# Performance work log

Hardware: AMD Instinct MI355X
Metric: run time of the kernel (lower is better)

The kernel has to match this reference:

```python
import jax, jax.numpy as jnp
import numpy as np
from jax import lax

K = 100
NUM_CLASSES = 80
MIN_X = 1; MIN_Y = 1; MAX_X = 4; MAX_Y = 4   # int(base_layer_range/16) for [16,64,16,64]
KEEP = 300
IOU_TH = 0.5
ROI_H = 2 * MAX_Y + 1  # 9
ROI_W = 2 * MAX_X + 1  # 9
MASK_OUT = 36          # 9 -> two stride-2 deconvs -> 36
SCALE = (36.0 - 1.0) / (9.0 - 1.0)
BN_INV = 1.0 / np.sqrt(1.0 + 1e-3)  # BN eval, running mean 0 / var 1, eps=1e-3
SIZES = [(64, 64), (32, 32), (16, 16)]


def bilinear(img, xx, yy):
    # img [..., H, W]; xx, yy same shape S; border-clamped bilinear sample -> [..., *S]
    H, W = img.shape[-2], img.shape[-1]
    xx = jnp.clip(xx, 0.0, W - 1.0)
    yy = jnp.clip(yy, 0.0, H - 1.0)
    x0f = jnp.floor(xx); y0f = jnp.floor(yy)
    wx = xx - x0f; wy = yy - y0f
    x0 = x0f.astype(jnp.int32); y0 = y0f.astype(jnp.int32)
    x1 = jnp.minimum(x0 + 1, W - 1); y1 = jnp.minimum(y0 + 1, H - 1)
    v00 = img[..., y0, x0]; v01 = img[..., y0, x1]
    v10 = img[..., y1, x0]; v11 = img[..., y1, x1]
    return (1 - wy) * ((1 - wx) * v00 + wx * v01) + wy * ((1 - wx) * v10 + wx * v11)


def roi_align(feat, boxes):
    # feat [C,H,W], boxes [N,4] in feat coords -> [N,C,ROI_H,ROI_W] (sampling_ratio=1)
    n = boxes.shape[0]
    x1, y1, x2, y2 = boxes[:, 0], boxes[:, 1], boxes[:, 2], boxes[:, 3]
    jx = (jnp.arange(ROI_W, dtype=jnp.float32) + 0.5) / ROI_W
    jy = (jnp.arange(ROI_H, dtype=jnp.float32) + 0.5) / ROI_H
    gx = x1[:, None] + (x2 - x1)[:, None] * jx  # [N,ROI_W]
    gy = y1[:, None] + (y2 - y1)[:, None] * jy  # [N,ROI_H]
    xx = jnp.broadcast_to(gx[:, None, :], (n, ROI_H, ROI_W))
    yy = jnp.broadcast_to(gy[:, :, None], (n, ROI_H, ROI_W))
    out = bilinear(feat, xx, yy)  # [C,N,ROI_H,ROI_W]
    return jnp.transpose(out, (1, 0, 2, 3))


def crop_resize(masks, boxes):
    # masks [N,h,w], boxes [N,4] -> [N,MASK_OUT,MASK_OUT]
    n = boxes.shape[0]
    t = jnp.arange(MASK_OUT, dtype=jnp.float32) / (MASK_OUT - 1.0)
    x1, y1, x2, y2 = boxes[:, 0], boxes[:, 1], boxes[:, 2], boxes[:, 3]
    gx = x1[:, None] + (x2 - x1)[:, None] * t
    gy = y1[:, None] + (y2 - y1)[:, None] * t
    xx = jnp.broadcast_to(gx[:, None, :], (n, MASK_OUT, MASK_OUT))
    yy = jnp.broadcast_to(gy[:, :, None], (n, MASK_OUT, MASK_OUT))
    return jax.vmap(bilinear)(masks, xx, yy)


def nms_keep(boxes, scores):
    # greedy NMS, faithful to torchvision semantics; returns bool keep flags [N]
    n = boxes.shape[0]
    x1, y1, x2, y2 = boxes[:, 0], boxes[:, 1], boxes[:, 2], boxes[:, 3]
    area = (x2 - x1) * (y2 - y1)
    ix1 = jnp.maximum(x1[:, None], x1[None, :]); iy1 = jnp.maximum(y1[:, None], y1[None, :])
    ix2 = jnp.minimum(x2[:, None], x2[None, :]); iy2 = jnp.minimum(y2[:, None], y2[None, :])
    inter = jnp.clip(ix2 - ix1, 0.0) * jnp.clip(iy2 - iy1, 0.0)
    iou = inter / (area[:, None] + area[None, :] - inter + 1e-9)
    order = jnp.argsort(-scores)  # stable
    def step(carry, idx):
        supp, keep = carry
        k = jnp.logical_not(supp[idx])
        keep = keep.at[idx].set(k)
        supp = jnp.logical_or(supp, jnp.logical_and(k, iou[idx] > IOU_TH))
        return (supp, keep), None
    init = (jnp.zeros((n,), bool), jnp.zeros((n,), bool))
    (_, keep), _ = lax.scan(step, init, order)
    return keep


def _conv(x, w, b, pad):
    y = lax.conv_general_dilated(x, w, (1, 1), [(pad, pad), (pad, pad)],
                                 dimension_numbers=('NCHW', 'OIHW', 'NCHW'))
    return y + b[None, :, None, None]


def _deconv(x, w, b):
    # ConvTranspose2d(k=2, s=2): fractionally-strided conv, doubles spatial size
    y = lax.conv_general_dilated(x, w, (1, 1), [(1, 1), (1, 1)], lhs_dilation=(2, 2),
                                 dimension_numbers=('NCHW', 'OIHW', 'NCHW'))
    return y + b[None, :, None, None]


def _bn(x, g, b):
    return x * (g * BN_INV)[None, :, None, None] + b[None, :, None, None]


def mask_head(x, c1_w, c1_b, mid_w, mid_b, bn_g, bn_b, d1_w, d1_b, d2_w, d2_b, c5_w, c5_b, c6_w, c6_b):
    r = jax.nn.relu
    h = r(_bn(_conv(x, c1_w, c1_b, 1), bn_g[0], bn_b[0]))
    for j in range(3):  # conv2..conv4
        h = r(_bn(_conv(h, mid_w[j], mid_b[j], 1), bn_g[1 + j], bn_b[1 + j]))
    h = r(_deconv(h, d1_w, d1_b))
    h = r(_bn(_conv(h, c5_w, c5_b, 1), bn_g[4], bn_b[4]))
    h = r(_deconv(h, d2_w, d2_b))
    return jax.nn.sigmoid(_conv(h, c6_w, c6_b, 0))


def _decode_layer(heat, tlr, brr, i, H0, W0):
    C, H, W = heat.shape
    hw = H * W
    scores, inds = lax.top_k(heat.reshape(-1), K)
    clses = (inds // hw).astype(jnp.float32)
    rem = inds % hw
    ys = (rem // W).astype(jnp.float32)
    xs = (rem % W).astype(jnp.float32)
    t = tlr.reshape(2, hw)[:, rem]  # [2,K]
    b = brr.reshape(2, hw)[:, rem]
    rx = float(MAX_X - MIN_X); ry = float(MAX_Y - MIN_Y)
    cx = (MAX_X + MIN_X) / 2.0;  cy = (MAX_Y + MIN_Y) / 2.0
    tlx = jnp.clip(xs - (rx * t[0] + cx), 0.0, float(W))
    tly = jnp.clip(ys - (ry * t[1] + cy), 0.0, float(H))
    brx = jnp.clip(xs + (rx * b[0] + cx), 0.0, float(W))
    bry = jnp.clip(ys + (ry * b[1] + cy), 0.0, float(H))
    boxes = jnp.stack([tlx, tly, brx, bry], 1)
    sc = jnp.where((brx < tlx) | (bry < tly), -1.0, scores)
    mb = jnp.stack([xs - MAX_X, ys - MAX_Y, xs + MAX_X, ys + MAX_Y,
                    jnp.full((K,), float(i))], 1)
    s2, order = lax.top_k(sc, K)  # num_dets(1000) >= K -> full sort by score
    boxes = boxes[order]; mb = mb[order]; cls = clses[order]
    lay = jnp.full((K,), float(i))
    cols = jnp.stack([s2, s2, lay, cls], 1)
    bws = jnp.concatenate([boxes, cols], 1)  # boxes_without_scaling [K,8]
    scale = jnp.array([W0 / W, H0 / H, W0 / W, H0 / H], jnp.float32)
    dets = jnp.concatenate([boxes * scale, cols], 1)
    return dets, bws, mb


def _decode_one(h0, h1, h2, t0, t1, t2, b0, b1, b2, f0, f1, f2,
                c1_w, c1_b, mid_w, mid_b, bn_g, bn_b, d1_w, d1_b, d2_w, d2_b,
                c5_w, c5_b, c6_w, c6_b):
    heats = (h0, h1, h2); tls = (t0, t1, t2); brs = (b0, b1, b2); feats = (f0, f1, f2)
    H0, W0 = heats[0].shape[1], heats[0].shape[2]
    dets_l, bws_l, mb_l = [], [], []
    for i in range(3):
        d, bw, mb = _decode_layer(heats[i], tls[i], brs[i], i, H0, W0)
        dets_l.append(d); bws_l.append(bw); mb_l.append(mb)
    dets = jnp.concatenate(dets_l, 0)   # [300,8]
    bws = jnp.concatenate(bws_l, 0)
    mb = jnp.concatenate(mb_l, 0)       # [300,5]
    # NMS faithful to source: boxes = detections[:,1:5], scores = detections[:,4]
    keep = nms_keep(dets[:, 1:5], dets[:, 4])
    sel = jnp.argsort(-jnp.where(keep, dets[:, 4], -1e9))[:KEEP]
    dets = dets[sel]; bws = bws[sel]; mb = mb[sel]
    # sort by mask layer index descending (features processed last->first)
    ord2 = jnp.argsort(-mb[:, 4])
    dets = dets[ord2]; bws = bws[ord2]; mb = mb[ord2]
    # ROI pool each box from its own layer's feature map
    pooled = jnp.stack([roi_align(feats[i], mb[:, :4]) for i in range(3)], 0)  # [3,N,C,9,9]
    lay = jnp.clip(mb[:, 4].astype(jnp.int32), 0, 2)
    rois = pooled[lay, jnp.arange(KEEP)]  # [N,256,9,9]
    masks_all = mask_head(rois, c1_w, c1_b, mid_w, mid_b, bn_g, bn_b,
                          d1_w, d1_b, d2_w, d2_b, c5_w, c5_b, c6_w, c6_b)  # [N,80,36,36]
    cls = jnp.clip(dets[:, 7].astype(jnp.int32), 0, NUM_CLASSES - 1)
    masks = masks_all[jnp.arange(KEEP), cls]  # [N,36,36] (one-hot scatter/select)
    bws4 = bws[:, :4] - jnp.tile(mb[:, :2], (1, 2))
    norm_boxes = SCALE * bws4
    masks = crop_resize(masks, norm_boxes)
    return dets, masks


def setup_inputs():
    key = jax.random.key(0)
    ks = jax.random.split(key, 32)
    B = 1
    inp = {}
    for i, (H, W) in enumerate(SIZES):
        inp['heat%d' % i] = jax.random.uniform(ks[i], (B, NUM_CLASSES, H, W), jnp.float32)
        inp['tl%d' % i] = 0.1 * jax.random.normal(ks[3 + i], (B, 2, H, W), jnp.float32)
        inp['br%d' % i] = 0.1 * jax.random.normal(ks[6 + i], (B, 2, H, W), jnp.float32)
        inp['feat%d' % i] = jax.random.normal(ks[9 + i], (B, 256, H, W), jnp.float32)
    inp['c1_w'] = 0.05 * jax.random.normal(ks[12], (256, 256, 3, 3), jnp.float32)
    inp['c1_b'] = jnp.zeros((256,), jnp.float32)
    inp['mid_w'] = 0.05 * jax.random.normal(ks[13], (3, 256, 256, 3, 3), jnp.float32)
    inp['mid_b'] = jnp.zeros((3, 256), jnp.float32)
    inp['bn_g'] = jnp.ones((5, 256), jnp.float32)
    inp['bn_b'] = jnp.zeros((5, 256), jnp.float32)
    inp['d1_w'] = 0.05 * jax.random.normal(ks[14], (256, 256, 2, 2), jnp.float32)
    inp['d1_b'] = jnp.zeros((256,), jnp.float32)
    inp['d2_w'] = 0.05 * jax.random.normal(ks[15], (256, 256, 2, 2), jnp.float32)
    inp['d2_b'] = jnp.zeros((256,), jnp.float32)
    inp['c5_w'] = 0.05 * jax.random.normal(ks[16], (256, 256, 3, 3), jnp.float32)
    inp['c5_b'] = jnp.zeros((256,), jnp.float32)
    inp['c6_w'] = 0.05 * jax.random.normal(ks[17], (NUM_CLASSES, 256, 1, 1), jnp.float32)
    inp['c6_b'] = jnp.zeros((NUM_CLASSES,), jnp.float32)
    return inp


def reference(heat0, heat1, heat2, tl0, tl1, tl2, br0, br1, br2, feat0, feat1, feat2,
              c1_w, c1_b, mid_w, mid_b, bn_g, bn_b, d1_w, d1_b, d2_w, d2_b,
              c5_w, c5_b, c6_w, c6_b):
    dets, masks = jax.vmap(_decode_one, in_axes=(0,) * 12 + (None,) * 14)(
        heat0, heat1, heat2, tl0, tl1, tl2, br0, br1, br2, feat0, feat1, feat2,
        c1_w, c1_b, mid_w, mid_b, bn_g, bn_b, d1_w, d1_b, d2_w, d2_b, c5_w, c5_b, c6_w, c6_b)
    return dets, masks  # [B,300,8], [B,300,36,36]
```

## Files before the change

### kernel.cpp

```cpp
#include <hip/hip_runtime.h>
#include <math.h>

typedef __attribute__((ext_vector_type(8))) short bf16x8;
typedef __attribute__((ext_vector_type(4))) float f32x4;

__device__ __forceinline__ unsigned fkey_u(float v){
  unsigned b = __float_as_uint(v);
  return (b & 0x80000000u) ? ~b : (b | 0x80000000u);
}
__device__ __forceinline__ float fkey_inv(unsigned m){
  unsigned b = (m & 0x80000000u) ? (m & 0x7fffffffu) : ~m;
  return __uint_as_float(b);
}
__device__ __forceinline__ unsigned short f2bf(float f){
  unsigned u = __float_as_uint(f);
  unsigned r = (u + 0x7fffu + ((u>>16)&1u)) >> 16;
  return (unsigned short)r;
}
__device__ __forceinline__ unsigned long long shfl_xor_u64(unsigned long long v, int mask){
  int lo = __shfl_xor((int)(unsigned)(v & 0xFFFFFFFFull), mask, 64);
  int hi = __shfl_xor((int)(unsigned)(v >> 32), mask, 64);
  return ((unsigned long long)(unsigned)hi << 32) | (unsigned long long)(unsigned)lo;
}
#define BNI 0.9995003746877732f

template<int E, int J>
__device__ __forceinline__ void reg_step(unsigned long long* key, int t, int k2){
  #pragma unroll
  for (int r=0;r<E;r++){
    if ((r & J)==0){
      int e = t*E + r;
      bool desc = ((e & k2)==0);
      unsigned long long a=key[r], b=key[r^J];
      if (desc ? (a<b) : (a>b)){ key[r]=b; key[r^J]=a; }
    }
  }
}
template<int E>
__device__ __forceinline__ void reg_tail(unsigned long long* key, int t, int k2, int jstart){
  if constexpr (E>=8) { if (jstart>=4) reg_step<E,4>(key,t,k2); }
  if constexpr (E>=4) { if (jstart>=2) reg_step<E,2>(key,t,k2); }
  if (jstart>=1) reg_step<E,1>(key,t,k2);
}
template<int E>
__device__ void bitonic_desc(unsigned long long* key, unsigned long long* lds){
  const int t = threadIdx.x;
  const int N = E*256;
  for (int k2=2;k2<=N;k2<<=1){
    for (int j=k2>>1; j>=E; j>>=1){
      int w = j/E;
      bool lower = ((t & w)==0);
      bool desc  = (((t*E) & k2)==0);
      bool keep_max = (desc == lower);
      if (w < 64){
        #pragma unroll
        for (int r=0;r<E;r++){
          unsigned long long mine=key[r];
          unsigned long long o=shfl_xor_u64(mine, w);
          bool gt = mine > o;
          key[r] = keep_max ? (gt?mine:o) : (gt?o:mine);
        }
      } else {
        __syncthreads();
        #pragma unroll
        for (int r=0;r<E;r++) lds[t*E+r]=key[r];
        __syncthreads();
        #pragma unroll
        for (int r=0;r<E;r++){
          unsigned long long mine=key[r];
          unsigned long long o=lds[(t*E+r)^j];
          bool gt = mine > o;
          key[r] = keep_max ? (gt?mine:o) : (gt?o:mine);
        }
      }
    }
    int jstart = ((k2>>1) < (E>>1)) ? (k2>>1) : (E>>1);
    reg_tail<E>(key,t,k2,jstart);
  }
  __syncthreads();
  #pragma unroll
  for (int r=0;r<E;r++) lds[t*E+r]=key[r];
  __syncthreads();
}

__global__ __launch_bounds__(256) void k_sel1(
    const float* __restrict__ h0, const float* __restrict__ h1, const float* __restrict__ h2,
    unsigned long long* __restrict__ c1)
{
  int b = blockIdx.x;
  int layer, chunk;
  if (b < 320){ layer=0; chunk=b; }
  else if (b < 400){ layer=1; chunk=b-320; }
  else { layer=2; chunk=b-400; }
  const float* heat = (layer==0)?h0:((layer==1)?h1:h2);
  __shared__ unsigned long long lds[1024];
  unsigned long long key[4];
  int t = threadIdx.x;
  int base = chunk*1024 + t*4;
  float4 v = *(const float4*)(heat + base);
  key[0] = ((unsigned long long)fkey_u(v.x)<<32) | (unsigned long long)(0xFFFFFFFFu - (unsigned)(base+0));
  key[1] = ((unsigned long long)fkey_u(v.y)<<32) | (unsigned long long)(0xFFFFFFFFu - (unsigned)(base+1));
  key[2] = ((unsigned long long)fkey_u(v.z)<<32) | (unsigned long long)(0xFFFFFFFFu - (unsigned)(base+2));
  key[3] = ((unsigned long long)fkey_u(v.w)<<32) | (unsigned long long)(0xFFFFFFFFu - (unsigned)(base+3));
  bitonic_desc<4>(key, lds);
  if (t<100) c1[(size_t)b*100 + t] = lds[t];
}

__global__ __launch_bounds__(256) void k_sel2(
    const unsigned long long* __restrict__ c1, unsigned long long* __restrict__ c2)
{
  int b = blockIdx.x;
  __shared__ unsigned long long lds[2048];
  unsigned long long key[8];
  int t=threadIdx.x;
  const unsigned long long* src = c1 + (size_t)b*2000;
  #pragma unroll
  for (int r=0;r<8;r++){
    int i=t*8+r;
    key[r] = (i<2000)? src[i] : 0ull;
  }
  bitonic_desc<8>(key, lds);
  if (t<100) c2[(size_t)b*100+t]=lds[t];
}

__global__ __launch_bounds__(256) void k_sel3_decode(
    const unsigned long long* __restrict__ c2,
    const float* __restrict__ tl0,const float* __restrict__ tl1,const float* __restrict__ tl2,
    const float* __restrict__ br0,const float* __restrict__ br1,const float* __restrict__ br2,
    float* __restrict__ dets, float* __restrict__ bws, float* __restrict__ mbw)
{
  int layer = blockIdx.x;
  int hw = 4096 >> (layer*2);
  int W = 64>>layer;
  float Wf = (float)W;
  const float* tl = (layer==0)?tl0:((layer==1)?tl1:tl2);
  const float* br = (layer==0)?br0:((layer==1)?br1:br2);
  int base = (layer==0)?0:((layer==1)?1600:2000);
  int cnt  = (layer==0)?1600:((layer==1)?400:100);
  __shared__ unsigned long long lds[2048];
  __shared__ float scl[100];
  unsigned long long key[8];
  int t = threadIdx.x;
  #pragma unroll
  for (int r=0;r<8;r++){
    int i=t*8+r;
    key[r] = (i<cnt)? c2[base+i] : 0ull;
  }
  bitonic_desc<8>(key, lds);
  unsigned long long kwin=0;
  if (t<100) kwin = lds[t];
  float tlx=0,tly=0,brx=0,bry=0,xs=0,ys=0,clsfv=0,scv=0;
  if (t<100){
    unsigned m=(unsigned)(kwin>>32);
    unsigned gidx = 0xFFFFFFFFu - (unsigned)(kwin & 0xFFFFFFFFull);
    float val = fkey_inv(m);
    int cls = (int)(gidx / (unsigned)hw);
    int rem = (int)(gidx % (unsigned)hw);
    int iy = rem / W, ix = rem % W;
    xs = (float)ix; ys = (float)iy; clsfv = (float)cls;
    float t0=tl[rem], t1=tl[hw+rem], b0=br[rem], b1=br[hw+rem];
    tlx = fminf(fmaxf(xs - (3.0f*t0 + 2.5f), 0.0f), Wf);
    tly = fminf(fmaxf(ys - (3.0f*t1 + 2.5f), 0.0f), Wf);
    brx = fminf(fmaxf(xs + (3.0f*b0 + 2.5f), 0.0f), Wf);
    bry = fminf(fmaxf(ys + (3.0f*b1 + 2.5f), 0.0f), Wf);
    scv = ((brx<tlx)||(bry<tly)) ? -1.0f : val;
    scl[t]=scv;
  }
  __syncthreads();
  if (t<100){
    int rank=0;
    for (int i=0;i<100;i++){
      float si=scl[i];
      rank += ((si>scv)||(si==scv && i<t)) ? 1 : 0;
    }
    int row = layer*100 + rank;
    float sx = (float)(1<<layer);
    float* dr = dets + row*8;
    dr[0]=tlx*sx; dr[1]=tly*sx; dr[2]=brx*sx; dr[3]=bry*sx;
    dr[4]=scv; dr[5]=scv; dr[6]=(float)layer; dr[7]=clsfv;
    float* bwr = bws + row*8;
    bwr[0]=tlx;bwr[1]=tly;bwr[2]=brx;bwr[3]=bry;bwr[4]=scv;bwr[5]=scv;bwr[6]=(float)layer;bwr[7]=clsfv;
    float* mr = mbw + row*5;
    mr[0]=xs-4.0f; mr[1]=ys-4.0f; mr[2]=xs+4.0f; mr[3]=ys+4.0f; mr[4]=(float)layer;
  }
}

#define SCAN_GROUP(SW, BASE, CNT) \
  _Pragma("unroll 4") \
  for (int rr=0; rr<CNT; rr++){ \
    int r = BASE+rr; \
    unsigned long long w0=sm[r][0],w1=sm[r][1],w2=sm[r][2],w3=sm[r][3],w4=sm[r][4]; \
    unsigned long long kq = (~(SW>>rr))&1ull; \
    keepr[r]=(unsigned char)kq; \
    unsigned long long msk = 0ull - kq; \
    s0|=w0&msk; s1|=w1&msk; s2|=w2&msk; s3|=w3&msk; s4|=w4&msk; \
  }

__global__ __launch_bounds__(320) void k_nms(
    const float* __restrict__ dets, const float* __restrict__ bws, const float* __restrict__ mbw,
    float* __restrict__ out_dets, float* __restrict__ mbf, int* __restrict__ clsf,
    int* __restrict__ layf, float* __restrict__ nbox)
{
  __shared__ __align__(16) float4 rb[300];
  __shared__ float rs[300];
  __shared__ int orig[300];
  __shared__ __align__(16) float sc[300];
  __shared__ __align__(16) float kk[300];
  __shared__ __align__(16) float lq[300];
  __shared__ float lyv[300];
  __shared__ unsigned long long sm[300][5];
  __shared__ unsigned char keepr[304];
  __shared__ int sel_[300], fperm[300];
  int t = threadIdx.x;
  float X1=0,Y1=0,X2=0,Y2=0,S=0;
  if (t<300){
    const float* r = dets + t*8;
    X1=r[1];Y1=r[2];X2=r[3];Y2=r[4];
    S=r[4];
    sc[t]=S;
    lyv[t]=mbw[t*5+4];
  }
  __syncthreads();
  if (t<300){
    int rank=0;
    for (int j4=0;j4<75;j4++){
      float4 s4=*(const float4*)&sc[j4*4];
      int j=j4*4;
      rank += ((s4.x>S)||(s4.x==S&&(j+0)<t)) ? 1:0;
      rank += ((s4.y>S)||(s4.y==S&&(j+1)<t)) ? 1:0;
      rank += ((s4.z>S)||(s4.z==S&&(j+2)<t)) ? 1:0;
      rank += ((s4.w>S)||(s4.w==S&&(j+3)<t)) ? 1:0;
    }
    rb[rank]=make_float4(X1,Y1,X2,Y2);
    rs[rank]=S;
    orig[rank]=t;
  }
  __syncthreads();
  if (t<300){
    float4 me=rb[t];
    float A=(me.z-me.x)*(me.w-me.y);
    #pragma unroll
    for (int jw=0;jw<5;jw++){
      unsigned long long bits=0;
      int lim=(jw==4)?44:64;
      for (int jj=0;jj<lim;jj++){
        int j=jw*64+jj;
        float4 q=rb[j];
        float aj=(q.z-q.x)*(q.w-q.y);
        float ix1=fmaxf(me.x,q.x), iy1=fmaxf(me.y,q.y);
        float ix2=fminf(me.z,q.z), iy2=fminf(me.w,q.w);
        float it=fmaxf(ix2-ix1,0.f)*fmaxf(iy2-iy1,0.f);
        float iou=it/(A+aj-it+1e-9f);
        bits |= ((unsigned long long)(iou>0.5f))<<jj;
      }
      sm[t][jw]=bits;
    }
  }
  __syncthreads();
  if (t==0){
    unsigned long long s0=0,s1=0,s2=0,s3=0,s4=0;
    SCAN_GROUP(s0,0,64)
    SCAN_GROUP(s1,64,64)
    SCAN_GROUP(s2,128,64)
    SCAN_GROUP(s3,192,64)
    SCAN_GROUP(s4,256,44)
  }
  __syncthreads();
  if (t<300) kk[orig[t]] = keepr[t] ? rs[t] : -1000000000.0f;
  __syncthreads();
  float KV=0; int rank2=0;
  if (t<300){
    KV=kk[t];
    for (int j4=0;j4<75;j4++){
      float4 s4=*(const float4*)&kk[j4*4];
      int j=j4*4;
      rank2 += ((s4.x>KV)||(s4.x==KV&&(j+0)<t)) ? 1:0;
      rank2 += ((s4.y>KV)||(s4.y==KV&&(j+1)<t)) ? 1:0;
      rank2 += ((s4.z>KV)||(s4.z==KV&&(j+2)<t)) ? 1:0;
      rank2 += ((s4.w>KV)||(s4.w==KV&&(j+3)<t)) ? 1:0;
    }
    sel_[rank2]=t;
  }
  __syncthreads();
  if (t<300) lq[t]=lyv[sel_[t]];
  __syncthreads();
  if (t<300){
    float L=lq[t]; int rank3=0;
    for (int j4=0;j4<75;j4++){
      float4 s4=*(const float4*)&lq[j4*4];
      int j=j4*4;
      rank3 += ((s4.x>L)||(s4.x==L&&(j+0)<t)) ? 1:0;
      rank3 += ((s4.y>L)||(s4.y==L&&(j+1)<t)) ? 1:0;
      rank3 += ((s4.z>L)||(s4.z==L&&(j+2)<t)) ? 1:0;
      rank3 += ((s4.w>L)||(s4.w==L&&(j+3)<t)) ? 1:0;
    }
    fperm[rank3]=sel_[t];
  }
  __syncthreads();
  if (t<300){
    int src=fperm[t];
    const float* dr=dets+src*8;
    #pragma unroll
    for (int c=0;c<8;c++) out_dets[t*8+c]=dr[c];
    const float* mr=mbw+src*5;
    #pragma unroll
    for (int c=0;c<5;c++) mbf[t*5+c]=mr[c];
    int cc=(int)dr[7]; cc = cc<0?0:(cc>79?79:cc); clsf[t]=cc;
    int lv=(int)mr[4]; lv = lv<0?0:(lv>2?2:lv); layf[t]=lv;
    const float* bw=bws+src*8;
    nbox[t*4+0]=4.375f*(bw[0]-mr[0]);
    nbox[t*4+1]=4.375f*(bw[1]-mr[1]);
    nbox[t*4+2]=4.375f*(bw[2]-mr[0]);
    nbox[t*4+3]=4.375f*(bw[3]-mr[1]);
  }
}

__global__ __launch_bounds__(256) void k_roi(
    const float* __restrict__ f0,const float* __restrict__ f1,const float* __restrict__ f2,
    const float* __restrict__ mbf, const int* __restrict__ layf,
    unsigned short* __restrict__ rois, int r0)
{
  int nl = blockIdx.x; int g = r0 + nl;
  __shared__ int ix0[9], ix1[9], iy0[9], iy1[9];
  __shared__ float wx[9], wy[9];
  int lay = layf[g];
  int W = 64>>lay;
  float Wf1 = (float)(W-1);
  const float* feat = (lay==0)?f0:((lay==1)?f1:f2);
  int t=threadIdx.x;
  if (t<9){
    float x1=mbf[g*5+0], x2=mbf[g*5+2];
    float jx = ((float)t + 0.5f)/9.0f;
    float gx = x1 + (x2-x1)*jx;
    float xx = fminf(fmaxf(gx,0.0f), Wf1);
    float x0f = floorf(xx);
    wx[t]=xx-x0f;
    int x0=(int)x0f; ix0[t]=x0; ix1[t]=min(x0+1,W-1);
  } else if (t>=16 && t<25){
    int j=t-16;
    float y1=mbf[g*5+1], y2=mbf[g*5+3];
    float jy=((float)j+0.5f)/9.0f;
    float gy=y1+(y2-y1)*jy;
    float yy=fminf(fmaxf(gy,0.0f),Wf1);
    float y0f=floorf(yy);
    wy[j]=yy-y0f;
    int y0=(int)y0f; iy0[j]=y0; iy1[j]=min(y0+1,W-1);
  }
  __syncthreads();
  int c=t;
  const float* fp = feat + (size_t)c*W*W;
  unsigned short* op = rois + (size_t)nl*81*256;
  for (int p=0;p<81;p++){
    int py=p/9, px=p%9;
    float v00=fp[iy0[py]*W+ix0[px]];
    float v01=fp[iy0[py]*W+ix1[px]];
    float v10=fp[iy1[py]*W+ix0[px]];
    float v11=fp[iy1[py]*W+ix1[px]];
    float wxx=wx[px], wyy=wy[py];
    float v = (1.0f-wyy)*((1.0f-wxx)*v00 + wxx*v01) + wyy*((1.0f-wxx)*v10 + wxx*v11);
    op[(size_t)p*256 + c] = f2bf(v);
  }
}

__global__ __launch_bounds__(64) void k_wprep3(
    const float* __restrict__ c1w, const float* __restrict__ midw, const float* __restrict__ c5w,
    unsigned short* __restrict__ WB)
{
  int b = blockIdx.x, c = blockIdx.y, l = threadIdx.x;
  int t = b>>7;
  const float* src = (c==0)? c1w : (c<=3 ? midw + (size_t)(c-1)*589824 : c5w);
  unsigned short* dst = WB + (size_t)c*589824 + ((size_t)b<<9) + l*8;
  int co = (b&15)*16 + (l&15);
  int cib = ((b>>4)&7)*32 + ((l>>4)<<3);
  #pragma unroll
  for (int j=0;j<8;j++) dst[j] = f2bf(src[((size_t)co*256 + cib + j)*9 + t]);
}
__global__ __launch_bounds__(64) void k_wprep2(
    const float* __restrict__ d1w, const float* __restrict__ d2w,
    unsigned short* __restrict__ WD)
{
  int b = blockIdx.x, c = blockIdx.y, l = threadIdx.x;
  int t = b>>7;
  const float* src = (c==0)? d1w : d2w;
  unsigned short* dst = WD + (size_t)c*262144 + ((size_t)b<<9) + l*8;
  int co = (b&15)*16 + (l&15);
  int cib = ((b>>4)&7)*32 + ((l>>4)<<3);
  #pragma unroll
  for (int j=0;j<8;j++) dst[j] = f2bf(src[((size_t)co*256 + cib + j)*4 + t]);
}

__global__ __launch_bounds__(256,3) void k_mconv9h(
    const unsigned short* __restrict__ Xg, unsigned short* __restrict__ Yg,
    const unsigned short* __restrict__ WBc,
    const float* __restrict__ Bc, const float* __restrict__ Gg, const float* __restrict__ Bn)
{
  __shared__ __align__(16) unsigned short Xp[88*264];
  int tid=threadIdx.x, l=tid&63, w=tid>>6;
  int h=blockIdx.y;
  int rlo = h ? 4 : -1;
  const unsigned short* Xr = Xg + (size_t)blockIdx.x*81*256;
  for (int idx=tid; idx<88*32; idx+=256){
    int pp=idx>>5, k8=idx&31;
    int y=pp/11 + rlo, x=pp%11 - 1;
    uint4 v{0,0,0,0};
    if ((unsigned)y<9u && (unsigned)x<9u) v = *(const uint4*)(Xr + ((y*9+x)<<8) + (k8<<3));
    *(uint4*)&Xp[pp*264 + (k8<<3)] = v;
  }
  __syncthreads();
  int mbase = h*48;
  int pixb[3];
  #pragma unroll
  for (int mt=0;mt<3;mt++){
    int m=mbase+mt*16+(l&15); if(m>80)m=80;
    pixb[mt]=(m/9 - rlo)*11 + (m%9) + 1;
  }
  int kg=(l>>4)<<3;
  f32x4 acc[3][4] = {};
  const unsigned short* wbase = WBc + (size_t)l*8;
  for (int t9=0;t9<9;t9++){
    int toff=(t9/3-1)*11 + (t9%3-1);
    for (int kc=0;kc<8;kc++){
      bf16x8 a[3], b[4];
      #pragma unroll
      for (int mt=0;mt<3;mt++) a[mt] = *(const bf16x8*)&Xp[(pixb[mt]+toff)*264 + (kc<<5) + kg];
      #pragma unroll
      for (int nn=0;nn<4;nn++) b[nn] = *(const bf16x8*)(wbase + ((size_t)(((t9<<3)+kc)*16 + (w<<2)+nn)<<9));
      #pragma unroll
      for (int mt=0;mt<3;mt++){
        #pragma unroll
        for (int nn=0;nn<4;nn++)
          acc[mt][nn] = __builtin_amdgcn_mfma_f32_16x16x32_bf16(a[mt], b[nn], acc[mt][nn], 0,0,0);
      }
    }
  }
  unsigned short* Yr = Yg + (size_t)blockIdx.x*81*256;
  int rb=(l>>4)<<2;
  #pragma unroll
  for (int nn=0;nn<4;nn++){
    int co=(w<<6)+(nn<<4)+(l&15);
    float bc=Bc[co], gm=Gg[co]*BNI, bb=Bn[co];
    #pragma unroll
    for (int mt=0;mt<3;mt++){
      #pragma unroll
      for (int r=0;r<4;r++){
        int m=mbase+mt*16+rb+r;
        if (m<81){
          float v=fmaxf((acc[mt][nn][r]+bc)*gm+bb, 0.f);
          Yr[m*256+co]=f2bf(v);
        }
      }
    }
  }
}

__global__ __launch_bounds__(256,3) void k_mdeconv1(
    const unsigned short* __restrict__ Xg, unsigned short* __restrict__ Yg,
    const unsigned short* __restrict__ WD1, const float* __restrict__ Bd)
{
  __shared__ __align__(16) unsigned short Xp[81*264];
  int tid=threadIdx.x, l=tid&63, w=tid>>6;
  int tp=blockIdx.y;
  const unsigned short* Xr = Xg + (size_t)blockIdx.x*81*256;
  for (int idx=tid; idx<81*32; idx+=256){
    int pp=idx>>5, k8=idx&31;
    *(uint4*)&Xp[pp*264+(k8<<3)] = *(const uint4*)(Xr + (pp<<8)+(k8<<3));
  }
  __syncthreads();
  int pixb[6];
  #pragma unroll
  for (int mt=0;mt<6;mt++){ int m=mt*16+(l&15); pixb[mt]=(m>80)?80:m; }
  int kg=(l>>4)<<3;
  f32x4 acc[6][4] = {};
  const unsigned short* wbase = WD1 + (size_t)tp*65536 + (size_t)l*8;
  for (int kc=0;kc<8;kc++){
    bf16x8 a[6], b[4];
    #pragma unroll
    for (int mt=0;mt<6;mt++) a[mt] = *(const bf16x8*)&Xp[pixb[mt]*264 + (kc<<5) + kg];
    #pragma unroll
    for (int nn=0;nn<4;nn++) b[nn] = *(const bf16x8*)(wbase + ((size_t)(kc*16 + (w<<2)+nn)<<9));
    #pragma unroll
    for (int mt=0;mt<6;mt++){
      #pragma unroll
      for (int nn=0;nn<4;nn++)
        acc[mt][nn] = __builtin_amdgcn_mfma_f32_16x16x32_bf16(a[mt], b[nn], acc[mt][nn], 0,0,0);
    }
  }
  unsigned short* Yr = Yg + (size_t)blockIdx.x*324*256;
  int ky=tp>>1, kx=tp&1;
  int rb=(l>>4)<<2;
  #pragma unroll
  for (int nn=0;nn<4;nn++){
    int co=(w<<6)+(nn<<4)+(l&15);
    float bd=Bd[co];
    #pragma unroll
    for (int mt=0;mt<6;mt++){
      #pragma unroll
      for (int r=0;r<4;r++){
        int m=mt*16+rb+r;
        if (m<81){
          int iy=m/9, ix=m%9;
          int opx=(2*iy+1-ky)*18 + (2*ix+1-kx);
          Yr[opx*256+co]=f2bf(fmaxf(acc[mt][nn][r]+bd,0.f));
        }
      }
    }
  }
}

__global__ __launch_bounds__(256,3) void k_mconv18(
    const unsigned short* __restrict__ Xg, unsigned short* __restrict__ Yg,
    const unsigned short* __restrict__ WBc,
    const float* __restrict__ Bc, const float* __restrict__ Gg, const float* __restrict__ Bn)
{
  __shared__ __align__(16) unsigned short Xp[160*136];
  int tid=threadIdx.x, l=tid&63, w=tid>>6;
  int rg=blockIdx.y, ch=blockIdx.z;
  const unsigned short* Xr = Xg + (size_t)blockIdx.x*324*256;
  int pixb[7];
  #pragma unroll
  for (int mt=0;mt<7;mt++){ int m=mt*16+(l&15); if(m>107)m=107; pixb[mt]=(m/18)*20+(m%18); }
  int kg=(l>>4)<<3;
  f32x4 acc[7][2] = {};
  const unsigned short* wbase = WBc + (size_t)l*8;
  for (int h=0;h<2;h++){
    __syncthreads();
    for (int idx=tid; idx<160*16; idx+=256){
      int pp=idx>>4, k8=idx&15;
      int py=rg*6-1+pp/20, px=pp%20-1;
      uint4 v{0,0,0,0};
      if ((unsigned)py<18u && (unsigned)px<18u)
        v = *(const uint4*)(Xr + ((py*18+px)<<8) + (h<<7) + (k8<<3));
      *(uint4*)&Xp[pp*136 + (k8<<3)] = v;
    }
    __syncthreads();
    for (int t9=0;t9<9;t9++){
      int toff=(t9/3)*20 + (t9%3);
      for (int kc=0;kc<4;kc++){
        int kcg=(h<<2)+kc;
        bf16x8 a[7], b[2];
        #pragma unroll
        for (int mt=0;mt<7;mt++) a[mt] = *(const bf16x8*)&Xp[(pixb[mt]+toff)*136 + (kc<<5) + kg];
        #pragma unroll
        for (int nn=0;nn<2;nn++) b[nn] = *(const bf16x8*)(wbase + ((size_t)(((t9<<3)+kcg)*16 + (ch<<3)+(w<<1)+nn)<<9));
        #pragma unroll
        for (int mt=0;mt<7;mt++){
          #pragma unroll
          for (int nn=0;nn<2;nn++)
            acc[mt][nn] = __builtin_amdgcn_mfma_f32_16x16x32_bf16(a[mt], b[nn], acc[mt][nn], 0,0,0);
        }
      }
    }
  }
  unsigned short* Yr = Yg + (size_t)blockIdx.x*324*256;
  int rb=(l>>4)<<2;
  #pragma unroll
  for (int nn=0;nn<2;nn++){
    int co=(ch<<7)+(w<<5)+(nn<<4)+(l&15);
    float bc=Bc[co], gm=Gg[co]*BNI, bb=Bn[co];
    #pragma unroll
    for (int mt=0;mt<7;mt++){
      #pragma unroll
      for (int r=0;r<4;r++){
        int m=mt*16+rb+r;
        if (m<108){
          int opx=rg*108+m;
          Yr[opx*256+co]=f2bf(fmaxf((acc[mt][nn][r]+bc)*gm+bb, 0.f));
        }
      }
    }
  }
}

__global__ __launch_bounds__(256,2) void k_mdec2c6(
    const unsigned short* __restrict__ Xg,
    const unsigned short* __restrict__ WD2, const float* __restrict__ Bd,
    const float* __restrict__ W6, const float* __restrict__ B6,
    const int* __restrict__ clsf, float* __restrict__ mask36, int r0)
{
  __shared__ __align__(16) unsigned short Xp[108*264];
  __shared__ float part[4][112];
  int tid=threadIdx.x, l=tid&63, w=tid>>6;
  int tp=blockIdx.y, rg=blockIdx.z;
  int g=r0+blockIdx.x;
  const unsigned short* Xr = Xg + (size_t)blockIdx.x*324*256 + (size_t)rg*108*256;
  for (int idx=tid; idx<108*32; idx+=256){
    int pp=idx>>5, k8=idx&31;
    *(uint4*)&Xp[pp*264+(k8<<3)] = *(const uint4*)(Xr + (pp<<8)+(k8<<3));
  }
  __syncthreads();
  int pixb[7];
  #pragma unroll
  for (int mt=0;mt<7;mt++){ int m=mt*16+(l&15); pixb[mt]=(m>107)?107:m; }
  int kg=(l>>4)<<3;
  f32x4 acc[7][4] = {};
  const unsigned short* wbase = WD2 + (size_t)tp*65536 + (size_t)l*8;
  for (int kc=0;kc<8;kc++){
    bf16x8 a[7], b[4];
    #pragma unroll
    for (int mt=0;mt<7;mt++) a[mt] = *(const bf16x8*)&Xp[pixb[mt]*264 + (kc<<5) + kg];
    #pragma unroll
    for (int nn=0;nn<4;nn++) b[nn] = *(const bf16x8*)(wbase + ((size_t)(kc*16 + (w<<2)+nn)<<9));
    #pragma unroll
    for (int mt=0;mt<7;mt++){
      #pragma unroll
      for (int nn=0;nn<4;nn++)
        acc[mt][nn] = __builtin_amdgcn_mfma_f32_16x16x32_bf16(a[mt], b[nn], acc[mt][nn], 0,0,0);
    }
  }
  int cls=clsf[g];
  float w6v[4], bdv[4];
  #pragma unroll
  for (int nn=0;nn<4;nn++){
    int co=(w<<6)+(nn<<4)+(l&15);
    w6v[nn]=W6[(size_t)cls*256+co];
    bdv[nn]=Bd[co];
  }
  int rb=(l>>4)<<2;
  #pragma unroll
  for (int mt=0;mt<7;mt++){
    float s0=0.f,s1=0.f,s2=0.f,s3=0.f;
    #pragma unroll
    for (int nn=0;nn<4;nn++){
      s0 += fmaxf(acc[mt][nn][0]+bdv[nn],0.f)*w6v[nn];
      s1 += fmaxf(acc[mt][nn][1]+bdv[nn],0.f)*w6v[nn];
      s2 += fmaxf(acc[mt][nn][2]+bdv[nn],0.f)*w6v[nn];
      s3 += fmaxf(acc[mt][nn][3]+bdv[nn],0.f)*w6v[nn];
    }
    #pragma unroll
    for (int o=1;o<16;o<<=1){
      s0 += __shfl_xor(s0,o,64);
      s1 += __shfl_xor(s1,o,64);
      s2 += __shfl_xor(s2,o,64);
      s3 += __shfl_xor(s3,o,64);
    }
    if ((l&15)==0){
      int mb=mt*16+rb;
      part[w][mb+0]=s0; part[w][mb+1]=s1; part[w][mb+2]=s2; part[w][mb+3]=s3;
    }
  }
  __syncthreads();
  if (tid<108){
    float lg = part[0][tid]+part[1][tid]+part[2][tid]+part[3][tid] + B6[cls];
    int pg=rg*108+tid, iy=pg/18, ix=pg%18;
    int ky=tp>>1, kx=tp&1;
    mask36[(size_t)g*1296 + (2*iy+1-ky)*36 + (2*ix+1-kx)] = 1.0f/(1.0f+expf(-lg));
  }
}

__global__ __launch_bounds__(256) void k_crop(
    const float* __restrict__ mask36, const float* __restrict__ nbox,
    float* __restrict__ outm)
{
  int r=blockIdx.x;
  __shared__ float m[1296];
  int t=threadIdx.x;
  for (int i=t;i<1296;i+=256) m[i]=mask36[(size_t)r*1296+i];
  float x1=nbox[r*4+0], y1=nbox[r*4+1], x2=nbox[r*4+2], y2=nbox[r*4+3];
  __syncthreads();
  for (int p=t;p<1296;p+=256){
    int oy=p/36, ox=p%36;
    float tx=(float)ox/35.0f, ty=(float)oy/35.0f;
    float gx=x1+(x2-x1)*tx, gy=y1+(y2-y1)*ty;
    float xx=fminf(fmaxf(gx,0.f),35.0f), yy=fminf(fmaxf(gy,0.f),35.0f);
    float x0f=floorf(xx), y0f=floorf(yy);
    float wxv=xx-x0f, wyv=yy-y0f;
    int x0=(int)x0f, y0=(int)y0f;
    int x1i=min(x0+1,35), y1i=min(y0+1,35);
    float v00=m[y0*36+x0], v01=m[y0*36+x1i], v10=m[y1i*36+x0], v11=m[y1i*36+x1i];
    outm[(size_t)r*1296+p]=(1.f-wyv)*((1.f-wxv)*v00+wxv*v01)+wyv*((1.f-wxv)*v10+wxv*v11);
  }
}

extern "C" void kernel_launch(void* const* d_in, const int* in_sizes, int n_in,
                              void* d_out, int out_size, void* d_ws, size_t ws_size,
                              hipStream_t stream) {
  int iH[3], iT[3], iB[3], iF[3];
  if (n_in >= 12 && in_sizes[1] == 2*64*64) {
    for (int l=0;l<3;l++){ iH[l]=l*4+0; iT[l]=l*4+1; iB[l]=l*4+2; iF[l]=l*4+3; }
  } else {
    for (int l=0;l<3;l++){ iH[l]=l; iT[l]=3+l; iB[l]=6+l; iF[l]=9+l; }
  }
  const float* heat0=(const float*)d_in[iH[0]];
  const float* heat1=(const float*)d_in[iH[1]];
  const float* heat2=(const float*)d_in[iH[2]];
  const float* tl0=(const float*)d_in[iT[0]];
  const float* tl1=(const float*)d_in[iT[1]];
  const float* tl2=(const float*)d_in[iT[2]];
  const float* br0=(const float*)d_in[iB[0]];
  const float* br1=(const float*)d_in[iB[1]];
  const float* br2=(const float*)d_in[iB[2]];
  const float* feat0=(const float*)d_in[iF[0]];
  const float* feat1=(const float*)d_in[iF[1]];
  const float* feat2=(const float*)d_in[iF[2]];
  const float* c1w=(const float*)d_in[12];
  const float* c1b=(const float*)d_in[13];
  const float* midw=(const float*)d_in[14];
  const float* midb=(const float*)d_in[15];
  const float* bng=(const float*)d_in[16];
  const float* bnb=(const float*)d_in[17];
  const float* d1w=(const float*)d_in[18];
  const float* d1b=(const float*)d_in[19];
  const float* d2w=(const float*)d_in[20];
  const float* d2b=(const float*)d_in[21];
  const float* c5w=(const float*)d_in[22];
  const float* c5b=(const float*)d_in[23];
  const float* c6w=(const float*)d_in[24];
  const float* c6b=(const float*)d_in[25];
  float* out=(float*)d_out;

  char* ws=(char*)d_ws;
  size_t cur=0;
  auto alloc=[&](size_t bytes)->char*{
    char* p=ws+cur;
    cur=(cur+bytes+255)&~(size_t)255;
    return p;
  };
  unsigned short* WB=(unsigned short*)alloc(5ull*589824*2);
  unsigned short* WD=(unsigned short*)alloc(2ull*262144*2);
  unsigned long long* c1s=(unsigned long long*)alloc(420ull*100*8);
  unsigned long long* c2s=(unsigned long long*)alloc(21ull*100*8);
  float* detsw=(float*)alloc(300*8*4);
  float* bwsw=(float*)alloc(300*8*4);
  float* mbw=(float*)alloc(300*5*4);
  float* mbf=(float*)alloc(300*5*4);
  int* clsf=(int*)alloc(300*4);
  int* layf=(int*)alloc(300*4);
  float* nbox=(float*)alloc(300*4*4);
  float* mask36=(float*)alloc(300ull*1296*4);
  size_t fixed=cur;
  size_t perroi = (size_t)(2*81 + 2*324)*256*2;
  size_t avail = (ws_size>fixed+4096)? (ws_size-fixed-4096):0;
  int NRC = (int)(avail/perroi);
  if (NRC>300) NRC=300;
  if (NRC<1) NRC=1;
  unsigned short* X0 =(unsigned short*)alloc((size_t)NRC*81*256*2);
  unsigned short* B9 =(unsigned short*)alloc((size_t)NRC*81*256*2);
  unsigned short* C18=(unsigned short*)alloc((size_t)NRC*324*256*2);
  unsigned short* D18=(unsigned short*)alloc((size_t)NRC*324*256*2);

  k_wprep3<<<dim3(1152,5),dim3(64),0,stream>>>(c1w,midw,c5w,WB);
  k_wprep2<<<dim3(512,2),dim3(64),0,stream>>>(d1w,d2w,WD);

  k_sel1<<<dim3(420),dim3(256),0,stream>>>(heat0,heat1,heat2,c1s);
  k_sel2<<<dim3(21),dim3(256),0,stream>>>(c1s,c2s);
  k_sel3_decode<<<dim3(3),dim3(256),0,stream>>>(c2s,tl0,tl1,tl2,br0,br1,br2,detsw,bwsw,mbw);
  k_nms<<<dim3(1),dim3(320),0,stream>>>(detsw,bwsw,mbw,out,mbf,clsf,layf,nbox);

  for (int r0=0;r0<300;r0+=NRC){
    int nr = (300-r0 < NRC)? (300-r0) : NRC;
    k_roi<<<dim3(nr),dim3(256),0,stream>>>(feat0,feat1,feat2,mbf,layf,X0,r0);
    k_mconv9h<<<dim3(nr,2),dim3(256),0,stream>>>(X0,B9,WB,               c1b,       bng,      bnb);
    k_mconv9h<<<dim3(nr,2),dim3(256),0,stream>>>(B9,X0,WB+1ull*589824,   midb,      bng+256,  bnb+256);
    k_mconv9h<<<dim3(nr,2),dim3(256),0,stream>>>(X0,B9,WB+2ull*589824,   midb+256,  bng+512,  bnb+512);
    k_mconv9h<<<dim3(nr,2),dim3(256),0,stream>>>(B9,X0,WB+3ull*589824,   midb+512,  bng+768,  bnb+768);
    k_mdeconv1<<<dim3(nr,4),dim3(256),0,stream>>>(X0,C18,WD,d1b);
    k_mconv18<<<dim3(nr,3,2),dim3(256),0,stream>>>(C18,D18,WB+4ull*589824, c5b, bng+1024, bnb+1024);
    k_mdec2c6<<<dim3(nr,4,3),dim3(256),0,stream>>>(D18,WD+262144,d2b,c6w,c6b,clsf,mask36,r0);
  }
  k_crop<<<dim3(300),dim3(256),0,stream>>>(mask36,nbox,out+2400);
}
```

Baseline: 657.0 us.

## Merge deconv tap and channel-half blocks, swizzle conv18 LDS tile

The deconv1 and deconv2+c6 kernels now loop over the four deconv taps inside one block instead of launching one block per tap, so the staged input tile in LDS is reused across taps. The 18x18 conv kernel drops its output-channel-half grid dimension so each block computes all 256 channels, with more accumulators per wave. Its LDS tile now uses an XOR swizzle on 16-byte chunks to reduce bank conflicts. The trade-off is fewer blocks (lower parallelism across the GPU) and higher register pressure from the larger accumulator array.

```diff
diff --git a/kernel.cpp b/kernel.cpp
--- a/kernel.cpp
+++ b/kernel.cpp
@@ -459,7 +459,6 @@
 {
   __shared__ __align__(16) unsigned short Xp[81*264];
   int tid=threadIdx.x, l=tid&63, w=tid>>6;
-  int tp=blockIdx.y;
   const unsigned short* Xr = Xg + (size_t)blockIdx.x*81*256;
   for (int idx=tid; idx<81*32; idx+=256){
     int pp=idx>>5, k8=idx&31;
@@ -470,37 +469,39 @@
   #pragma unroll
   for (int mt=0;mt<6;mt++){ int m=mt*16+(l&15); pixb[mt]=(m>80)?80:m; }
   int kg=(l>>4)<<3;
-  f32x4 acc[6][4] = {};
-  const unsigned short* wbase = WD1 + (size_t)tp*65536 + (size_t)l*8;
-  for (int kc=0;kc<8;kc++){
-    bf16x8 a[6], b[4];
+  int rb=(l>>4)<<2;
+  unsigned short* Yr = Yg + (size_t)blockIdx.x*324*256;
+  for (int tp=0;tp<4;tp++){
+    f32x4 acc[6][4] = {};
+    const unsigned short* wbase = WD1 + (size_t)tp*65536 + (size_t)l*8;
+    for (int kc=0;kc<8;kc++){
+      bf16x8 a[6], b[4];
+      #pragma unroll
+      for (int mt=0;mt<6;mt++) a[mt] = *(const bf16x8*)&Xp[pixb[mt]*264 + (kc<<5) + kg];
+      #pragma unroll
+      for (int nn=0;nn<4;nn++) b[nn] = *(const bf16x8*)(wbase + ((size_t)(kc*16 + (w<<2)+nn)<<9));
+      #pragma unroll
+      for (int mt=0;mt<6;mt++){
+        #pragma unroll
+        for (int nn=0;nn<4;nn++)
+          acc[mt][nn] = __builtin_amdgcn_mfma_f32_16x16x32_bf16(a[mt], b[nn], acc[mt][nn], 0,0,0);
+      }
+    }
+    int ky=tp>>1, kx=tp&1;
     #pragma unroll
-    for (int mt=0;mt<6;mt++) a[mt] = *(const bf16x8*)&Xp[pixb[mt]*264 + (kc<<5) + kg];
-    #pragma unroll
-    for (int nn=0;nn<4;nn++) b[nn] = *(const bf16x8*)(wbase + ((size_t)(kc*16 + (w<<2)+nn)<<9));
-    #pragma unroll
-    for (int mt=0;mt<6;mt++){
-      #pragma unroll
-      for (int nn=0;nn<4;nn++)
-        acc[mt][nn] = __builtin_amdgcn_mfma_f32_16x16x32_bf16(a[mt], b[nn], acc[mt][nn], 0,0,0);
-    }
-  }
-  unsigned short* Yr = Yg + (size_t)blockIdx.x*324*256;
-  int ky=tp>>1, kx=tp&1;
-  int rb=(l>>4)<<2;
-  #pragma unroll
-  for (int nn=0;nn<4;nn++){
-    int co=(w<<6)+(nn<<4)+(l&15);
-    float bd=Bd[co];
-    #pragma unroll
-    for (int mt=0;mt<6;mt++){
-      #pragma unroll
-      for (int r=0;r<4;r++){
-        int m=mt*16+rb+r;
-        if (m<81){
-          int iy=m/9, ix=m%9;
-          int opx=(2*iy+1-ky)*18 + (2*ix+1-kx);
-          Yr[opx*256+co]=f2bf(fmaxf(acc[mt][nn][r]+bd,0.f));
+    for (int nn=0;nn<4;nn++){
+      int co=(w<<6)+(nn<<4)+(l&15);
+      float bd=Bd[co];
+      #pragma unroll
+      for (int mt=0;mt<6;mt++){
+        #pragma unroll
+        for (int r=0;r<4;r++){
+          int m=mt*16+rb+r;
+          if (m<81){
+            int iy=m/9, ix=m%9;
+            int opx=(2*iy+1-ky)*18 + (2*ix+1-kx);
+            Yr[opx*256+co]=f2bf(fmaxf(acc[mt][nn][r]+bd,0.f));
+          }
         }
       }
     }
@@ -514,13 +515,13 @@
 {
   __shared__ __align__(16) unsigned short Xp[160*136];
   int tid=threadIdx.x, l=tid&63, w=tid>>6;
-  int rg=blockIdx.y, ch=blockIdx.z;
+  int rg=blockIdx.y;
   const unsigned short* Xr = Xg + (size_t)blockIdx.x*324*256;
   int pixb[7];
   #pragma unroll
   for (int mt=0;mt<7;mt++){ int m=mt*16+(l&15); if(m>107)m=107; pixb[mt]=(m/18)*20+(m%18); }
-  int kg=(l>>4)<<3;
-  f32x4 acc[7][2] = {};
+  int g16=l>>4;
+  f32x4 acc[7][4] = {};
   const unsigned short* wbase = WBc + (size_t)l*8;
   for (int h=0;h<2;h++){
     __syncthreads();
@@ -530,22 +531,26 @@
       uint4 v{0,0,0,0};
       if ((unsigned)py<18u && (unsigned)px<18u)
         v = *(const uint4*)(Xr + ((py*18+px)<<8) + (h<<7) + (k8<<3));
-      *(uint4*)&Xp[pp*136 + (k8<<3)] = v;
+      *(uint4*)&Xp[pp*136 + ((k8 ^ (pp&7))<<3)] = v;
     }
     __syncthreads();
     for (int t9=0;t9<9;t9++){
       int toff=(t9/3)*20 + (t9%3);
       for (int kc=0;kc<4;kc++){
         int kcg=(h<<2)+kc;
-        bf16x8 a[7], b[2];
-        #pragma unroll
-        for (int mt=0;mt<7;mt++) a[mt] = *(const bf16x8*)&Xp[(pixb[mt]+toff)*136 + (kc<<5) + kg];
-        #pragma unroll
-        for (int nn=0;nn<2;nn++) b[nn] = *(const bf16x8*)(wbase + ((size_t)(((t9<<3)+kcg)*16 + (ch<<3)+(w<<1)+nn)<<9));
+        bf16x8 a[7], b[4];
+        #pragma unroll
+        for (int mt=0;mt<7;mt++){
+          int row=pixb[mt]+toff;
+          int gg=((kc<<2)+g16) ^ (row&7);
+          a[mt] = *(const bf16x8*)&Xp[row*136 + (gg<<3)];
+        }
+        #pragma unroll
+        for (int nn=0;nn<4;nn++) b[nn] = *(const bf16x8*)(wbase + ((size_t)(((t9<<3)+kcg)*16 + (w<<2)+nn)<<9));
         #pragma unroll
         for (int mt=0;mt<7;mt++){
           #pragma unroll
-          for (int nn=0;nn<2;nn++)
+          for (int nn=0;nn<4;nn++)
             acc[mt][nn] = __builtin_amdgcn_mfma_f32_16x16x32_bf16(a[mt], b[nn], acc[mt][nn], 0,0,0);
         }
       }
@@ -554,8 +559,8 @@
   unsigned short* Yr = Yg + (size_t)blockIdx.x*324*256;
   int rb=(l>>4)<<2;
   #pragma unroll
-  for (int nn=0;nn<2;nn++){
-    int co=(ch<<7)+(w<<5)+(nn<<4)+(l&15);
+  for (int nn=0;nn<4;nn++){
+    int co=(w<<6)+(nn<<4)+(l&15);
     float bc=Bc[co], gm=Gg[co]*BNI, bb=Bn[co];
     #pragma unroll
     for (int mt=0;mt<7;mt++){
@@ -580,7 +585,7 @@
   __shared__ __align__(16) unsigned short Xp[108*264];
   __shared__ float part[4][112];
   int tid=threadIdx.x, l=tid&63, w=tid>>6;
-  int tp=blockIdx.y, rg=blockIdx.z;
+  int rg=blockIdx.y;
   int g=r0+blockIdx.x;
   const unsigned short* Xr = Xg + (size_t)blockIdx.x*324*256 + (size_t)rg*108*256;
   for (int idx=tid; idx<108*32; idx+=256){
@@ -592,21 +597,7 @@
   #pragma unroll
   for (int mt=0;mt<7;mt++){ int m=mt*16+(l&15); pixb[mt]=(m>107)?107:m; }
   int kg=(l>>4)<<3;
-  f32x4 acc[7][4] = {};
-  const unsigned short* wbase = WD2 + (size_t)tp*65536 + (size_t)l*8;
-  for (int kc=0;kc<8;kc++){
-    bf16x8 a[7], b[4];
-    #pragma unroll
-    for (int mt=0;mt<7;mt++) a[mt] = *(const bf16x8*)&Xp[pixb[mt]*264 + (kc<<5) + kg];
-    #pragma unroll
-    for (int nn=0;nn<4;nn++) b[nn] = *(const bf16x8*)(wbase + ((size_t)(kc*16 + (w<<2)+nn)<<9));
-    #pragma unroll
-    for (int mt=0;mt<7;mt++){
-      #pragma unroll
-      for (int nn=0;nn<4;nn++)
-        acc[mt][nn] = __builtin_amdgcn_mfma_f32_16x16x32_bf16(a[mt], b[nn], acc[mt][nn], 0,0,0);
-    }
-  }
+  int rb=(l>>4)<<2;
   int cls=clsf[g];
   float w6v[4], bdv[4];
   #pragma unroll
@@ -615,35 +606,53 @@
     w6v[nn]=W6[(size_t)cls*256+co];
     bdv[nn]=Bd[co];
   }
-  int rb=(l>>4)<<2;
-  #pragma unroll
-  for (int mt=0;mt<7;mt++){
-    float s0=0.f,s1=0.f,s2=0.f,s3=0.f;
+  float b6c=B6[cls];
+  for (int tp=0;tp<4;tp++){
+    f32x4 acc[7][4] = {};
+    const unsigned short* wbase = WD2 + (size_t)tp*65536 + (size_t)l*8;
+    for (int kc=0;kc<8;kc++){
+      bf16x8 a[7], b[4];
+      #pragma unroll
+      for (int mt=0;mt<7;mt++) a[mt] = *(const bf16x8*)&Xp[pixb[mt]*264 + (kc<<5) + kg];
+      #pragma unroll
+      for (int nn=0;nn<4;nn++) b[nn] = *(const bf16x8*)(wbase + ((size_t)(kc*16 + (w<<2)+nn)<<9));
+      #pragma unroll
+      for (int mt=0;mt<7;mt++){
+        #pragma unroll
+        for (int nn=0;nn<4;nn++)
+          acc[mt][nn] = __builtin_amdgcn_mfma_f32_16x16x32_bf16(a[mt], b[nn], acc[mt][nn], 0,0,0);
+      }
+    }
     #pragma unroll
-    for (int nn=0;nn<4;nn++){
-      s0 += fmaxf(acc[mt][nn][0]+bdv[nn],0.f)*w6v[nn];
-      s1 += fmaxf(acc[mt][nn][1]+bdv[nn],0.f)*w6v[nn];
-      s2 += fmaxf(acc[mt][nn][2]+bdv[nn],0.f)*w6v[nn];
-      s3 += fmaxf(acc[mt][nn][3]+bdv[nn],0.f)*w6v[nn];
-    }
-    #pragma unroll
-    for (int o=1;o<16;o<<=1){
-      s0 += __shfl_xor(s0,o,64);
-      s1 += __shfl_xor(s1,o,64);
-      s2 += __shfl_xor(s2,o,64);
-      s3 += __shfl_xor(s3,o,64);
-    }
-    if ((l&15)==0){
-      int mb=mt*16+rb;
-      part[w][mb+0]=s0; part[w][mb+1]=s1; part[w][mb+2]=s2; part[w][mb+3]=s3;
-    }
-  }
-  __syncthreads();
-  if (tid<108){
-    float lg = part[0][tid]+part[1][tid]+part[2][tid]+part[3][tid] + B6[cls];
-    int pg=rg*108+tid, iy=pg/18, ix=pg%18;
-    int ky=tp>>1, kx=tp&1;
-    mask36[(size_t)g*1296 + (2*iy+1-ky)*36 + (2*ix+1-kx)] = 1.0f/(1.0f+expf(-lg));
+    for (int mt=0;mt<7;mt++){
+      float s0=0.f,s1=0.f,s2=0.f,s3=0.f;
+      #pragma unroll
+      for (int nn=0;nn<4;nn++){
+        s0 += fmaxf(acc[mt][nn][0]+bdv[nn],0.f)*w6v[nn];
+        s1 += fmaxf(acc[mt][nn][1]+bdv[nn],0.f)*w6v[nn];
+        s2 += fmaxf(acc[mt][nn][2]+bdv[nn],0.f)*w6v[nn];
+        s3 += fmaxf(acc[mt][nn][3]+bdv[nn],0.f)*w6v[nn];
+      }
+      #pragma unroll
+      for (int o=1;o<16;o<<=1){
+        s0 += __shfl_xor(s0,o,64);
+        s1 += __shfl_xor(s1,o,64);
+        s2 += __shfl_xor(s2,o,64);
+        s3 += __shfl_xor(s3,o,64);
+      }
+      if ((l&15)==0){
+        int mb=mt*16+rb;
+        part[w][mb+0]=s0; part[w][mb+1]=s1; part[w][mb+2]=s2; part[w][mb+3]=s3;
+      }
+    }
+    __syncthreads();
+    if (tid<108){
+      float lg = part[0][tid]+part[1][tid]+part[2][tid]+part[3][tid] + b6c;
+      int pg=rg*108+tid, iy=pg/18, ix=pg%18;
+      int ky=tp>>1, kx=tp&1;
+      mask36[(size_t)g*1296 + (2*iy+1-ky)*36 + (2*ix+1-kx)] = 1.0f/(1.0f+expf(-lg));
+    }
+    __syncthreads();
   }
 }
 
@@ -753,9 +762,9 @@
     k_mconv9h<<<dim3(nr,2),dim3(256),0,stream>>>(B9,X0,WB+1ull*589824,   midb,      bng+256,  bnb+256);
     k_mconv9h<<<dim3(nr,2),dim3(256),0,stream>>>(X0,B9,WB+2ull*589824,   midb+256,  bng+512,  bnb+512);
     k_mconv9h<<<dim3(nr,2),dim3(256),0,stream>>>(B9,X0,WB+3ull*589824,   midb+512,  bng+768,  bnb+768);
-    k_mdeconv1<<<dim3(nr,4),dim3(256),0,stream>>>(X0,C18,WD,d1b);
-    k_mconv18<<<dim3(nr,3,2),dim3(256),0,stream>>>(C18,D18,WB+4ull*589824, c5b, bng+1024, bnb+1024);
-    k_mdec2c6<<<dim3(nr,4,3),dim3(256),0,stream>>>(D18,WD+262144,d2b,c6w,c6b,clsf,mask36,r0);
+    k_mdeconv1<<<dim3(nr),dim3(256),0,stream>>>(X0,C18,WD,d1b);
+    k_mconv18<<<dim3(nr,3),dim3(256),0,stream>>>(C18,D18,WB+4ull*589824, c5b, bng+1024, bnb+1024);
+    k_mdec2c6<<<dim3(nr,3),dim3(256),0,stream>>>(D18,WD+262144,d2b,c6w,c6b,clsf,mask36,r0);
   }
   k_crop<<<dim3(300),dim3(256),0,stream>>>(mask36,nbox,out+2400);
 }
```

After: 669.4 us. Within noise of the previous version (+1.9%).
